# Performance work log

Measured on AMD Instinct MI355X. Metric: run time of the kernel, lower is better.

The kernel has to match this reference:

```python
import jax, jax.numpy as jnp
import numpy as np

RES = 128        # 2**base_lod, base_lod=7, num_lod=1
FEAT_DIM = 18


def setup_inputs() -> dict:
    key = jax.random.key(0)
    k1, k2 = jax.random.split(key)
    pts = jax.random.uniform(k1, (4, 524288, 3), dtype=jnp.float32)
    codebook = jax.random.normal(k2, (RES ** 3, FEAT_DIM), dtype=jnp.float32) * 0.01
    transform = jnp.eye(4, dtype=jnp.float32)
    return {"pts": pts, "codebook": codebook, "transform": transform}


def _trilinear(res, codebook, pts):
    # pts: [N,3] in [0,1]; NGLOD-style dense grid trilinear interpolation
    p = pts * (res - 1)
    p0 = jnp.floor(p)
    w = p - p0                                   # [N,3] fractional weights
    i0 = jnp.clip(p0.astype(jnp.int32), 0, res - 1)
    i1 = jnp.clip(i0 + 1, 0, res - 1)
    feats = jnp.zeros((pts.shape[0], codebook.shape[1]), dtype=codebook.dtype)
    for dz in (0, 1):
        iz = (i1 if dz else i0)[:, 2]
        wz = w[:, 2] if dz else 1.0 - w[:, 2]
        for dy in (0, 1):
            iy = (i1 if dy else i0)[:, 1]
            wy = w[:, 1] if dy else 1.0 - w[:, 1]
            for dx in (0, 1):
                ix = (i1 if dx else i0)[:, 0]
                wx = w[:, 0] if dx else 1.0 - w[:, 0]
                idx = ix + iy * res + iz * res * res   # x + y*res + z*res^2
                feats = feats + codebook[idx] * (wx * wy * wz)[:, None]
    return feats


def reference(pts, codebook, transform):
    # flatten 'b h c -> (b h) c'
    p = pts.reshape(-1, 3)
    R_inv = jnp.linalg.inv(transform[:3, :3])
    p = (R_inv @ (p.T - transform[:3, 3:4])).T
    feats = _trilinear(RES, codebook, p)
    # single LOD: cat over lod axis then sum(-1) is identity
    return feats
```

## Files before the change

### kernel.cpp

```cpp
#include <hip/hip_runtime.h>


constexpr int RES = 128;
constexpr int TPB = 576;
constexpr int PPB = TPB / 9;

typedef float vf2 __attribute__((ext_vector_type(2)));

__global__ __launch_bounds__(TPB)
void dense_grid_trilerp(const float* __restrict__ pts,
                        const float* __restrict__ cb,
                        const float* __restrict__ tr,
                        float* __restrict__ out,
                        int npts)
{
    __shared__ float spts[PPB * 3];
    if (threadIdx.x < PPB * 3) {
        int g = blockIdx.x * (PPB * 3) + threadIdx.x;
        spts[threadIdx.x] = (g < npts * 3) ? __builtin_nontemporal_load(&pts[g]) : 0.0f;
    }
    __syncthreads();

    const int pl = threadIdx.x / 9;
    const int f  = threadIdx.x - pl * 9;
    const int p  = blockIdx.x * PPB + pl;
    if (p >= npts) return;

    const float a = tr[0], b = tr[1],  c = tr[2],  tx = tr[3];
    const float d = tr[4], e = tr[5],  g_ = tr[6], ty = tr[7];
    const float h = tr[8], i_ = tr[9], j = tr[10], tz = tr[11];
    const float det = a*(e*j - g_*i_) - b*(d*j - g_*h) + c*(d*i_ - e*h);
    const float rd  = 1.0f / det;
    const float m00 = (e*j - g_*i_) * rd, m01 = (c*i_ - b*j) * rd, m02 = (b*g_ - c*e) * rd;
    const float m10 = (g_*h - d*j) * rd,  m11 = (a*j - c*h) * rd,  m12 = (c*d - a*g_) * rd;
    const float m20 = (d*i_ - e*h) * rd,  m21 = (b*h - a*i_) * rd, m22 = (a*e - b*d) * rd;

    const float x = spts[pl*3 + 0] - tx;
    const float y = spts[pl*3 + 1] - ty;
    const float z = spts[pl*3 + 2] - tz;
    const float qx = (m00*x + m01*y + m02*z) * (float)(RES - 1);
    const float qy = (m10*x + m11*y + m12*z) * (float)(RES - 1);
    const float qz = (m20*x + m21*y + m22*z) * (float)(RES - 1);

    const float fx = floorf(qx), fy = floorf(qy), fz = floorf(qz);
    const float wx1 = qx - fx, wy1 = qy - fy, wz1 = qz - fz;
    const float wx0 = 1.0f - wx1, wy0 = 1.0f - wy1, wz0 = 1.0f - wz1;
    const int ix0 = min(max((int)fx, 0), RES - 1); const int ix1 = min(ix0 + 1, RES - 1);
    const int iy0 = min(max((int)fy, 0), RES - 1); const int iy1 = min(iy0 + 1, RES - 1);
    const int iz0 = min(max((int)fz, 0), RES - 1); const int iz1 = min(iz0 + 1, RES - 1);

    int   ro[8];
    float w[8];
    #pragma unroll
    for (int k = 0; k < 8; ++k) {
        const int dx = k & 1, dy = (k >> 1) & 1, dz = k >> 2;
        const int ix = dx ? ix1 : ix0;
        const int iy = dy ? iy1 : iy0;
        const int iz = dz ? iz1 : iz0;
        ro[k] = ix + (iy << 7) + (iz << 14);
        w[k]  = (dx ? wx1 : wx0) * (dy ? wy1 : wy0) * (dz ? wz1 : wz0);
    }

    const float* cbf = cb + 2 * f;
    vf2 v[8];
    #pragma unroll
    for (int k = 0; k < 8; ++k)
        v[k] = *reinterpret_cast<const vf2*>(cbf + ro[k] * 18);

    float ax = 0.0f, ay = 0.0f;
    #pragma unroll
    for (int k = 0; k < 8; ++k) { ax += v[k].x * w[k]; ay += v[k].y * w[k]; }

    vf2 r; r.x = ax; r.y = ay;
    __builtin_nontemporal_store(r, reinterpret_cast<vf2*>(out + p * 18 + 2 * f));
}

extern "C" void kernel_launch(void* const* d_in, const int* in_sizes, int n_in,
                              void* d_out, int out_size, void* d_ws, size_t ws_size,
                              hipStream_t stream) {
    const float* pts = (const float*)d_in[0];
    const float* cb  = (const float*)d_in[1];
    const float* tr  = (const float*)d_in[2];
    float* out = (float*)d_out;

    const int npts   = in_sizes[0] / 3;
    const int blocks = (npts + PPB - 1) / PPB;
    dense_grid_trilerp<<<blocks, TPB, 0, stream>>>(pts, cb, tr, out, npts);
}
```

Before: 511.7 us.

## Bin points spatially by z/y slab before gathering codebook entries

Adds a counting-sort preprocessing pipeline (histogram, scan, scatter) that groups points into 512 bins keyed by z cell and coarse y, storing transformed coordinates plus the original index. The main gather kernel then processes points in bin order, so neighbouring blocks touch nearby codebook rows and cache locality improves for the random 151 MB codebook. In exchange it adds four extra launches, atomics, and a 16-byte-per-point record write and read, and output stores become scattered by original index.

```diff
diff --git a/kernel.cpp b/kernel.cpp
--- a/kernel.cpp
+++ b/kernel.cpp
@@ -2,22 +2,148 @@
 
 
 constexpr int RES = 128;
+constexpr int NB  = 512;
 constexpr int TPB = 576;
 constexpr int PPB = TPB / 9;
 
+constexpr int HIST_CHUNK = 1024;
+constexpr int SCAT_CHUNK = 4096;
+
 typedef float vf2 __attribute__((ext_vector_type(2)));
+typedef float vf4 __attribute__((ext_vector_type(4)));
+
+struct Xf {
+    float m00, m01, m02, m10, m11, m12, m20, m21, m22;
+    float tx, ty, tz;
+};
+
+__device__ __forceinline__ Xf load_xf(const float* __restrict__ tr) {
+    Xf X;
+    const float a = tr[0], b = tr[1],  c = tr[2];
+    const float d = tr[4], e = tr[5],  g = tr[6];
+    const float h = tr[8], i = tr[9],  j = tr[10];
+    X.tx = tr[3]; X.ty = tr[7]; X.tz = tr[11];
+    const float det = a*(e*j - g*i) - b*(d*j - g*h) + c*(d*i - e*h);
+    const float rd  = 1.0f / det;
+    X.m00 = (e*j - g*i) * rd; X.m01 = (c*i - b*j) * rd; X.m02 = (b*g - c*e) * rd;
+    X.m10 = (g*h - d*j) * rd; X.m11 = (a*j - c*h) * rd; X.m12 = (c*d - a*g) * rd;
+    X.m20 = (d*i - e*h) * rd; X.m21 = (b*h - a*i) * rd; X.m22 = (a*e - b*d) * rd;
+    return X;
+}
+
+__device__ __forceinline__ float qcoord(float m0, float m1, float m2,
+                                        float x, float y, float z) {
+    return __fmaf_rn(m0, x, __fmaf_rn(m1, y, m2 * z)) * (float)(RES - 1);
+}
+
+__device__ __forceinline__ int bin_of(const Xf& X, float x, float y, float z) {
+    const float qy = qcoord(X.m10, X.m11, X.m12, x, y, z);
+    const float qz = qcoord(X.m20, X.m21, X.m22, x, y, z);
+    const int iy0 = min(max((int)floorf(qy), 0), RES - 1);
+    const int iz0 = min(max((int)floorf(qz), 0), RES - 1);
+    return (iz0 << 2) + (iy0 >> 5);
+}
+
+__global__ __launch_bounds__(NB)
+void k_zero(unsigned* __restrict__ hist) {
+    hist[threadIdx.x] = 0u;
+}
+
+__global__ __launch_bounds__(256)
+void k_hist(const float* __restrict__ pts, const float* __restrict__ tr,
+            unsigned* __restrict__ hist, int npts)
+{
+    __shared__ unsigned sh[NB];
+    for (int b = threadIdx.x; b < NB; b += 256) sh[b] = 0u;
+    __syncthreads();
+    const Xf X = load_xf(tr);
+    const int base = blockIdx.x * HIST_CHUNK;
+    #pragma unroll
+    for (int i = 0; i < HIST_CHUNK / 256; ++i) {
+        const int p = base + threadIdx.x + i * 256;
+        if (p < npts) {
+            const float x = pts[p*3 + 0] - X.tx;
+            const float y = pts[p*3 + 1] - X.ty;
+            const float z = pts[p*3 + 2] - X.tz;
+            atomicAdd(&sh[bin_of(X, x, y, z)], 1u);
+        }
+    }
+    __syncthreads();
+    for (int b = threadIdx.x; b < NB; b += 256) {
+        const unsigned c = sh[b];
+        if (c) atomicAdd(&hist[b], c);
+    }
+}
+
+__global__ __launch_bounds__(NB)
+void k_scan(const unsigned* __restrict__ hist, unsigned* __restrict__ cursor)
+{
+    __shared__ unsigned s[NB];
+    const int t = threadIdx.x;
+    const unsigned my = hist[t];
+    s[t] = my;
+    __syncthreads();
+    for (int off = 1; off < NB; off <<= 1) {
+        const unsigned v = (t >= off) ? s[t - off] : 0u;
+        __syncthreads();
+        s[t] += v;
+        __syncthreads();
+    }
+    cursor[t] = s[t] - my;
+}
+
+__global__ __launch_bounds__(256)
+void k_scatter(const float* __restrict__ pts, const float* __restrict__ tr,
+               unsigned* __restrict__ cursor, vf4* __restrict__ rec, int npts)
+{
+    __shared__ unsigned shist[NB], sbase[NB], scur[NB];
+    const int t = threadIdx.x;
+    for (int b = t; b < NB; b += 256) { shist[b] = 0u; scur[b] = 0u; }
+    __syncthreads();
+    const Xf X = load_xf(tr);
+    const int base = blockIdx.x * SCAT_CHUNK;
+    #pragma unroll
+    for (int i = 0; i < SCAT_CHUNK / 256; ++i) {
+        const int p = base + t + i * 256;
+        if (p < npts) {
+            const float x = pts[p*3 + 0] - X.tx;
+            const float y = pts[p*3 + 1] - X.ty;
+            const float z = pts[p*3 + 2] - X.tz;
+            atomicAdd(&shist[bin_of(X, x, y, z)], 1u);
+        }
+    }
+    __syncthreads();
+    for (int b = t; b < NB; b += 256)
+        sbase[b] = atomicAdd(&cursor[b], shist[b]);
+    __syncthreads();
+    #pragma unroll
+    for (int i = 0; i < SCAT_CHUNK / 256; ++i) {
+        const int p = base + t + i * 256;
+        if (p < npts) {
+            const float x = pts[p*3 + 0] - X.tx;
+            const float y = pts[p*3 + 1] - X.ty;
+            const float z = pts[p*3 + 2] - X.tz;
+            const float qx = qcoord(X.m00, X.m01, X.m02, x, y, z);
+            const float qy = qcoord(X.m10, X.m11, X.m12, x, y, z);
+            const float qz = qcoord(X.m20, X.m21, X.m22, x, y, z);
+            const int bn = bin_of(X, x, y, z);
+            const unsigned r = atomicAdd(&scur[bn], 1u);
+            unsigned pos = sbase[bn] + r;
+            if (pos >= (unsigned)npts) pos = (unsigned)npts - 1u;
+            vf4 v; v.x = qx; v.y = qy; v.z = qz; v.w = __int_as_float(p);
+            rec[pos] = v;
+        }
+    }
+}
 
 __global__ __launch_bounds__(TPB)
-void dense_grid_trilerp(const float* __restrict__ pts,
-                        const float* __restrict__ cb,
-                        const float* __restrict__ tr,
-                        float* __restrict__ out,
-                        int npts)
-{
-    __shared__ float spts[PPB * 3];
-    if (threadIdx.x < PPB * 3) {
-        int g = blockIdx.x * (PPB * 3) + threadIdx.x;
-        spts[threadIdx.x] = (g < npts * 3) ? __builtin_nontemporal_load(&pts[g]) : 0.0f;
+void k_main(const vf4* __restrict__ rec, const float* __restrict__ cb,
+            float* __restrict__ out, int npts)
+{
+    __shared__ vf4 srec[PPB];
+    if (threadIdx.x < PPB) {
+        const int g = blockIdx.x * PPB + threadIdx.x;
+        if (g < npts) srec[threadIdx.x] = rec[g];
     }
     __syncthreads();
 
@@ -26,21 +152,9 @@
     const int p  = blockIdx.x * PPB + pl;
     if (p >= npts) return;
 
-    const float a = tr[0], b = tr[1],  c = tr[2],  tx = tr[3];
-    const float d = tr[4], e = tr[5],  g_ = tr[6], ty = tr[7];
-    const float h = tr[8], i_ = tr[9], j = tr[10], tz = tr[11];
-    const float det = a*(e*j - g_*i_) - b*(d*j - g_*h) + c*(d*i_ - e*h);
-    const float rd  = 1.0f / det;
-    const float m00 = (e*j - g_*i_) * rd, m01 = (c*i_ - b*j) * rd, m02 = (b*g_ - c*e) * rd;
-    const float m10 = (g_*h - d*j) * rd,  m11 = (a*j - c*h) * rd,  m12 = (c*d - a*g_) * rd;
-    const float m20 = (d*i_ - e*h) * rd,  m21 = (b*h - a*i_) * rd, m22 = (a*e - b*d) * rd;
-
-    const float x = spts[pl*3 + 0] - tx;
-    const float y = spts[pl*3 + 1] - ty;
-    const float z = spts[pl*3 + 2] - tz;
-    const float qx = (m00*x + m01*y + m02*z) * (float)(RES - 1);
-    const float qy = (m10*x + m11*y + m12*z) * (float)(RES - 1);
-    const float qz = (m20*x + m21*y + m22*z) * (float)(RES - 1);
+    const vf4 r = srec[pl];
+    const float qx = r.x, qy = r.y, qz = r.z;
+    const int idx = __float_as_int(r.w);
 
     const float fx = floorf(qx), fy = floorf(qy), fz = floorf(qz);
     const float wx1 = qx - fx, wy1 = qy - fy, wz1 = qz - fz;
@@ -71,8 +185,68 @@
     #pragma unroll
     for (int k = 0; k < 8; ++k) { ax += v[k].x * w[k]; ay += v[k].y * w[k]; }
 
-    vf2 r; r.x = ax; r.y = ay;
-    __builtin_nontemporal_store(r, reinterpret_cast<vf2*>(out + p * 18 + 2 * f));
+    vf2 o; o.x = ax; o.y = ay;
+    __builtin_nontemporal_store(o, reinterpret_cast<vf2*>(out + idx * 18 + 2 * f));
+}
+
+__global__ __launch_bounds__(TPB)
+void dense_grid_trilerp(const float* __restrict__ pts,
+                        const float* __restrict__ cb,
+                        const float* __restrict__ tr,
+                        float* __restrict__ out,
+                        int npts)
+{
+    __shared__ float spts[PPB * 3];
+    if (threadIdx.x < PPB * 3) {
+        int g = blockIdx.x * (PPB * 3) + threadIdx.x;
+        spts[threadIdx.x] = (g < npts * 3) ? __builtin_nontemporal_load(&pts[g]) : 0.0f;
+    }
+    __syncthreads();
+
+    const int pl = threadIdx.x / 9;
+    const int f  = threadIdx.x - pl * 9;
+    const int p  = blockIdx.x * PPB + pl;
+    if (p >= npts) return;
+
+    const Xf X = load_xf(tr);
+    const float x = spts[pl*3 + 0] - X.tx;
+    const float y = spts[pl*3 + 1] - X.ty;
+    const float z = spts[pl*3 + 2] - X.tz;
+    const float qx = qcoord(X.m00, X.m01, X.m02, x, y, z);
+    const float qy = qcoord(X.m10, X.m11, X.m12, x, y, z);
+    const float qz = qcoord(X.m20, X.m21, X.m22, x, y, z);
+
+    const float fx = floorf(qx), fy = floorf(qy), fz = floorf(qz);
+    const float wx1 = qx - fx, wy1 = qy - fy, wz1 = qz - fz;
+    const float wx0 = 1.0f - wx1, wy0 = 1.0f - wy1, wz0 = 1.0f - wz1;
+    const int ix0 = min(max((int)fx, 0), RES - 1); const int ix1 = min(ix0 + 1, RES - 1);
+    const int iy0 = min(max((int)fy, 0), RES - 1); const int iy1 = min(iy0 + 1, RES - 1);
+    const int iz0 = min(max((int)fz, 0), RES - 1); const int iz1 = min(iz0 + 1, RES - 1);
+
+    int   ro[8];
+    float w[8];
+    #pragma unroll
+    for (int k = 0; k < 8; ++k) {
+        const int dx = k & 1, dy = (k >> 1) & 1, dz = k >> 2;
+        const int ix = dx ? ix1 : ix0;
+        const int iy = dy ? iy1 : iy0;
+        const int iz = dz ? iz1 : iz0;
+        ro[k] = ix + (iy << 7) + (iz << 14);
+        w[k]  = (dx ? wx1 : wx0) * (dy ? wy1 : wy0) * (dz ? wz1 : wz0);
+    }
+
+    const float* cbf = cb + 2 * f;
+    vf2 v[8];
+    #pragma unroll
+    for (int k = 0; k < 8; ++k)
+        v[k] = *reinterpret_cast<const vf2*>(cbf + ro[k] * 18);
+
+    float ax = 0.0f, ay = 0.0f;
+    #pragma unroll
+    for (int k = 0; k < 8; ++k) { ax += v[k].x * w[k]; ay += v[k].y * w[k]; }
+
+    vf2 o; o.x = ax; o.y = ay;
+    __builtin_nontemporal_store(o, reinterpret_cast<vf2*>(out + p * 18 + 2 * f));
 }
 
 extern "C" void kernel_launch(void* const* d_in, const int* in_sizes, int n_in,
@@ -83,7 +257,22 @@
     const float* tr  = (const float*)d_in[2];
     float* out = (float*)d_out;
 
-    const int npts   = in_sizes[0] / 3;
-    const int blocks = (npts + PPB - 1) / PPB;
-    dense_grid_trilerp<<<blocks, TPB, 0, stream>>>(pts, cb, tr, out, npts);
-}
+    const int npts = in_sizes[0] / 3;
+
+    const size_t need = (size_t)NB * 2 * sizeof(unsigned) + (size_t)npts * 16 + 256;
+    if (d_ws == nullptr || ws_size < need || npts <= 0) {
+        const int blocks = (npts + PPB - 1) / PPB;
+        dense_grid_trilerp<<<blocks, TPB, 0, stream>>>(pts, cb, tr, out, npts);
+        return;
+    }
+
+    unsigned* hist   = (unsigned*)d_ws;
+    unsigned* cursor = hist + NB;
+    vf4* rec = (vf4*)((char*)d_ws + ((size_t)NB * 2 * sizeof(unsigned) + 255) / 256 * 256);
+
+    k_zero<<<1, NB, 0, stream>>>(hist);
+    k_hist<<<(npts + HIST_CHUNK - 1) / HIST_CHUNK, 256, 0, stream>>>(pts, tr, hist, npts);
+    k_scan<<<1, NB, 0, stream>>>(hist, cursor);
+    k_scatter<<<(npts + SCAT_CHUNK - 1) / SCAT_CHUNK, 256, 0, stream>>>(pts, tr, cursor, rec, npts);
+    k_main<<<(npts + PPB - 1) / PPB, TPB, 0, stream>>>(rec, cb, out, npts);
+}
```

After: 506.5 us. No clear change (-1.0%).
